# Optimization experiments

Hardware: AMD Instinct MI355X
Metric: run time of the kernel (lower is better)

## Reference

```python
import jax, jax.numpy as jnp
import numpy as np

B, N, M = 8, 1024, 64          # graphs, ops/graph, machines/graph
OPF, MF = 16, 8                # raw feature dims
H, D, L = 8, 64, 3             # heads, head dim, HGT layers
F = H * D                      # 512 = hidden_dim * num_heads
KC = 8                         # compatible machines per op
NOP, NM = B * N, B * M
EPS = 1e-5


def _graph_ln(x, w, b):
    # PyG LayerNorm(mode='graph') with batch=None: scalar mean/std over the whole tensor
    x = x - x.mean()
    return x / (x.std() + EPS) * w + b


def _seg_softmax(a, idx, n):
    amax = jax.ops.segment_max(a, idx, num_segments=n)
    amax = jnp.where(jnp.isfinite(amax), amax, 0.0)
    ex = jnp.exp(a - amax[idx])
    s = jax.ops.segment_sum(ex, idx, num_segments=n)
    return ex / (s[idx] + 1e-16)


def _forward(op_x, machine_x, W_emb_op, b_emb_op, W_emb_m, b_emb_m,
             opn_w, opn_b, mn_w, mn_b, Wk, bk, Wq, bq, Wv, bv,
             A_rel, M_rel, p_rel, W_out, b_out, skip, ln_w, ln_b,
             ei_precedes, ei_canproc, ei_compat):
    x_op = _graph_ln(op_x @ W_emb_op + b_emb_op, opn_w, opn_b)
    x_m = _graph_ln(machine_x @ W_emb_m + b_emb_m, mn_w, mn_b)
    s0, d0 = ei_precedes   # op -> op
    s1, d1 = ei_canproc    # machine -> op
    s2, d2 = ei_compat     # op -> machine
    scale = 1.0 / jnp.sqrt(jnp.float32(D))
    for l in range(L):
        k_op = (x_op @ Wk[l, 0] + bk[l, 0]).reshape(NOP, H, D)
        q_op = (x_op @ Wq[l, 0] + bq[l, 0]).reshape(NOP, H, D)
        v_op = (x_op @ Wv[l, 0] + bv[l, 0]).reshape(NOP, H, D)
        k_m = (x_m @ Wk[l, 1] + bk[l, 1]).reshape(NM, H, D)
        q_m = (x_m @ Wq[l, 1] + bq[l, 1]).reshape(NM, H, D)
        v_m = (x_m @ Wv[l, 1] + bv[l, 1]).reshape(NM, H, D)
        # relation-specific per-head transforms (a_rel/m_rel of HGTConv)
        k0 = jnp.einsum('nhd,hde->nhe', k_op, A_rel[l, 0]); v0 = jnp.einsum('nhd,hde->nhe', v_op, M_rel[l, 0])
        k1 = jnp.einsum('nhd,hde->nhe', k_m, A_rel[l, 1]);  v1 = jnp.einsum('nhd,hde->nhe', v_m, M_rel[l, 1])
        k2 = jnp.einsum('nhd,hde->nhe', k_op, A_rel[l, 2]); v2 = jnp.einsum('nhd,hde->nhe', v_op, M_rel[l, 2])
        # attention into op nodes: joint softmax over both incoming edge types
        a0 = (q_op[d0] * k0[s0]).sum(-1) * p_rel[l, 0] * scale   # [E0,H]
        a1 = (q_op[d1] * k1[s1]).sum(-1) * p_rel[l, 1] * scale   # [E1,H]
        a_op = jnp.concatenate([a0, a1]); dd = jnp.concatenate([d0, d1])
        w = _seg_softmax(a_op, dd, NOP)
        msg = jnp.concatenate([v0[s0], v1[s1]]) * w[:, :, None]
        agg_op = jax.ops.segment_sum(msg, dd, num_segments=NOP).reshape(NOP, F)
        # attention into machine nodes
        a2 = (q_m[d2] * k2[s2]).sum(-1) * p_rel[l, 2] * scale
        w2 = _seg_softmax(a2, d2, NM)
        agg_m = jax.ops.segment_sum(v2[s2] * w2[:, :, None], d2, num_segments=NM).reshape(NM, F)
        # output projection + learned skip gate (HGTConv internals)
        o_op = jax.nn.gelu(agg_op, approximate=False) @ W_out[l, 0] + b_out[l, 0]
        o_m = jax.nn.gelu(agg_m, approximate=False) @ W_out[l, 1] + b_out[l, 1]
        g_op = jax.nn.sigmoid(skip[l, 0]); g_m = jax.nn.sigmoid(skip[l, 1])
        o_op = g_op * o_op + (1.0 - g_op) * x_op
        o_m = g_m * o_m + (1.0 - g_m) * x_m
        # wrapper residual + dropout(eval=identity) + graph layer norm
        x_op = _graph_ln(o_op + x_op, ln_w[l], ln_b[l])
        x_m = _graph_ln(o_m + x_m, ln_w[l], ln_b[l])
    fea_j = x_op.reshape(B, N, F)
    fea_m = x_m.reshape(B, M, F)
    return fea_j, fea_m, fea_j.mean(1, keepdims=True), fea_m.mean(1, keepdims=True)


def setup_inputs() -> dict:
    key = jax.random.key(0)
    ks = jax.random.split(key, 12)
    rng = np.random.default_rng(0)
    ids = np.arange(NOP).reshape(B, N)
    src0 = ids[:, :-1].ravel(); dst0 = ids[:, 1:].ravel()
    mach = rng.integers(0, M, size=(B, N, KC)) + (np.arange(B) * M)[:, None, None]
    ops = np.broadcast_to(ids[:, :, None], (B, N, KC))
    ei_precedes = jnp.asarray(np.stack([src0, dst0]), dtype=jnp.int32)
    ei_canproc = jnp.asarray(np.stack([mach.ravel(), ops.ravel()]), dtype=jnp.int32)
    ei_compat = jnp.asarray(np.stack([ops.ravel(), mach.ravel()]), dtype=jnp.int32)
    n = lambda k, sh, s=0.05: jax.random.normal(k, sh, dtype=jnp.float32) * s
    return dict(
        op_x=n(ks[0], (NOP, OPF), 1.0),
        machine_x=n(ks[1], (NM, MF), 1.0),
        W_emb_op=n(ks[2], (OPF, F)), b_emb_op=jnp.zeros((F,), jnp.float32),
        W_emb_m=n(ks[3], (MF, F)), b_emb_m=jnp.zeros((F,), jnp.float32),
        opn_w=jnp.ones((F,), jnp.float32), opn_b=jnp.zeros((F,), jnp.float32),
        mn_w=jnp.ones((F,), jnp.float32), mn_b=jnp.zeros((F,), jnp.float32),
        Wk=n(ks[4], (L, 2, F, F)), bk=jnp.zeros((L, 2, F), jnp.float32),
        Wq=n(ks[5], (L, 2, F, F)), bq=jnp.zeros((L, 2, F), jnp.float32),
        Wv=n(ks[6], (L, 2, F, F)), bv=jnp.zeros((L, 2, F), jnp.float32),
        A_rel=n(ks[7], (L, 3, H, D, D)), M_rel=n(ks[8], (L, 3, H, D, D)),
        p_rel=jnp.ones((L, 3, H), jnp.float32),
        W_out=n(ks[9], (L, 2, F, F)), b_out=jnp.zeros((L, 2, F), jnp.float32),
        skip=jnp.ones((L, 2), jnp.float32),
        ln_w=jnp.ones((L, F), jnp.float32), ln_b=jnp.zeros((L, F), jnp.float32),
        ei_precedes=ei_precedes, ei_canproc=ei_canproc, ei_compat=ei_compat,
    )


def reference(op_x, machine_x, W_emb_op, b_emb_op, W_emb_m, b_emb_m,
              opn_w, opn_b, mn_w, mn_b, Wk, bk, Wq, bq, Wv, bv,
              A_rel, M_rel, p_rel, W_out, b_out, skip, ln_w, ln_b,
              ei_precedes, ei_canproc, ei_compat):
    return _forward(op_x, machine_x, W_emb_op, b_emb_op, W_emb_m, b_emb_m,
                    opn_w, opn_b, mn_w, mn_b, Wk, bk, Wq, bq, Wv, bv,
                    A_rel, M_rel, p_rel, W_out, b_out, skip, ln_w, ln_b,
                    ei_precedes, ei_canproc, ei_compat)
```

## Files before the change

kernel.cpp:

```cpp
#include <hip/hip_runtime.h>

typedef unsigned short u16;
typedef __attribute__((ext_vector_type(4))) float floatx4;
typedef __attribute__((ext_vector_type(8))) short shortx8;
typedef __attribute__((ext_vector_type(4))) short shortx4;

#define NOPS 8192
#define NMS  512
#define CQ   2560
#define CM   1536
#define NE2  65536
#define TOPC (NOPS*512)
#define TMC  (NMS*512)

__device__ __forceinline__ float bf2f(u16 u){ return __uint_as_float(((unsigned)u)<<16); }
__device__ __forceinline__ u16 f2bf(float f){
  unsigned u = __float_as_uint(f);
  u += 0x7FFFu + ((u>>16)&1u);
  return (u16)(u>>16);
}
__device__ __forceinline__ float wred(float v){
  #pragma unroll
  for (int o=32;o;o>>=1) v += __shfl_xor(v,o,64);
  return v;
}
__device__ __forceinline__ float wredmax(float v){
  #pragma unroll
  for (int o=32;o;o>>=1) v = fmaxf(v, __shfl_xor(v,o,64));
  return v;
}
__device__ __forceinline__ float geluf(float x){
  return 0.5f*x*(1.f+erff(x*0.70710678118654752f));
}
__device__ __forceinline__ void block_stat_out2(float s, float s2, float* pstat, int slot){
  __shared__ float sb[8];
  s = wred(s); s2 = wred(s2);
  int wv = threadIdx.x >> 6;
  if ((threadIdx.x & 63) == 0){ sb[wv*2] = s; sb[wv*2+1] = s2; }
  __syncthreads();
  if (threadIdx.x == 0){
    float a = 0.f, b = 0.f;
    int nw = blockDim.x >> 6;
    for (int i=0;i<nw;++i){ a += sb[i*2]; b += sb[i*2+1]; }
    pstat[slot*2]   = a;
    pstat[slot*2+1] = b;
  }
}

__global__ __launch_bounds__(256) void cnt2_k(const int* __restrict__ s1, float* __restrict__ Ct,
                                              float* __restrict__ Cn){
  int idx = blockIdx.x*256 + threadIdx.x;
  int n = idx >> 6, l = idx & 63;
  const int* row = s1 + n*8;
  int cnt = 0;
  #pragma unroll
  for (int j=0;j<8;++j) cnt += ((row[j] & 63) == l);
  float f = (float)cnt;
  Cn[(size_t)n*64 + l] = f;
  int b = n >> 10, nl = n & 1023;
  Ct[(size_t)((b<<6) + l)*1024 + nl] = f;
}

__global__ __launch_bounds__(256) void twout_k(const float* __restrict__ src, u16* __restrict__ dst){
  __shared__ u16 t[64][65];
  int l = blockIdx.x, kb = blockIdx.y*64, nb = blockIdx.z*64;
  const float* s = src + (size_t)l*262144;
  u16* d = dst + (size_t)l*262144;
  int tx = threadIdx.x & 63, ty4 = threadIdx.x >> 6;
  #pragma unroll 4
  for (int p=0;p<16;++p){
    int k = ty4 + p*4;
    t[k][tx] = f2bf(s[(size_t)(kb+k)*512 + nb + tx]);
  }
  __syncthreads();
  #pragma unroll 4
  for (int p=0;p<16;++p){
    int n = ty4 + p*4;
    d[(size_t)(nb+n)*512 + kb + tx] = t[tx][n];
  }
}

__global__ __launch_bounds__(256) void tq_k(const float* __restrict__ Wq,
                                            u16* __restrict__ Wc_op_t, u16* __restrict__ Wc_m_t){
  __shared__ u16 tl[64][65];
  int blk = blockIdx.x;
  int l = blk >> 1, side = blk & 1;
  const float* s = Wq + (size_t)blk*262144;
  u16* d = side ? (Wc_m_t + (size_t)l*CM*512) : (Wc_op_t + (size_t)l*CQ*512);
  int kb = blockIdx.y*64, nb = blockIdx.z*64;
  int tx = threadIdx.x & 63, ty4 = threadIdx.x >> 6;
  #pragma unroll 4
  for (int p=0;p<16;++p){
    int k = ty4 + p*4;
    tl[k][tx] = f2bf(s[(size_t)(kb+k)*512 + nb + tx]);
  }
  __syncthreads();
  #pragma unroll 4
  for (int p=0;p<16;++p){
    int n = ty4 + p*4;
    d[(size_t)(nb+n)*512 + kb + tx] = tl[tx][n];
  }
}

__global__ void qb_k(const float* __restrict__ bq, float* bias_op, float* bias_m){
  int i = blockIdx.x*blockDim.x + threadIdx.x;
  if (i >= 3072) return;
  int l = i >> 10, side = (i >> 9) & 1, f = i & 511;
  float v = bq[(l*2+side)*512 + f];
  if (side==0) bias_op[l*CQ + f] = v; else bias_m[l*CM + f] = v;
}

__global__ __launch_bounds__(256) void combine3_k(const float* __restrict__ Wk, const float* __restrict__ Wv,
                                                  const float* __restrict__ Ar, const float* __restrict__ Mr,
                                                  u16* __restrict__ Wc_op_t, u16* __restrict__ Wc_m_t){
  __shared__ u16 As[64*72];
  __shared__ u16 Bs[128*72];
  int gx = blockIdx.x;
  int l = gx/48; int rem = gx - l*48; int s = rem >> 3; int h = rem & 7;
  int side = (s < 4) ? 0 : 1;
  int r = (s < 4) ? (s+1) : (s-3);
  int useK = side==0 ? (s==0 || s==2) : (s==4);
  int rel  = side==0 ? ((s<2)?0:2) : 1;
  const float* W   = (useK ? Wk : Wv) + (size_t)(l*2+side)*262144;
  const float* Rel = (useK ? Ar : Mr) + ((size_t)(l*3+rel)*8 + h)*4096;
  int h64 = h*64;
  u16* Wt = side ? (Wc_m_t + (size_t)l*CM*512) : (Wc_op_t + (size_t)l*CQ*512);
  int rbase = r*512 + h64;
  int cc0 = blockIdx.y * 128;
  int tid = threadIdx.x, lane = tid & 63, wave = tid >> 6;
  {
    int d = tid >> 2, e0 = (tid & 3) * 16;
    #pragma unroll
    for (int j=0;j<16;++j) As[(e0+j)*72 + d] = f2bf(Rel[d*64 + e0 + j]);
  }
  {
    int ccl = tid >> 1, d0 = (tid & 1) * 32;
    const float* src = W + (size_t)(cc0+ccl)*512 + h64 + d0;
    #pragma unroll
    for (int j=0;j<32;j+=4){
      floatx4 v = *(const floatx4*)(src + j);
      shortx4 sv;
      #pragma unroll
      for (int e=0;e<4;++e) sv[e] = (short)f2bf(v[e]);
      *(shortx4*)(Bs + ccl*72 + d0 + j) = sv;
    }
  }
  __syncthreads();
  int wm = wave & 1, wn = wave >> 1;
  int mrow = lane & 15, quad = lane >> 4;
  floatx4 acc[2][4];
  #pragma unroll
  for (int a=0;a<2;++a)
    #pragma unroll
    for (int b=0;b<4;++b) acc[a][b] = (floatx4){0.f,0.f,0.f,0.f};
  #pragma unroll
  for (int ks=0; ks<2; ++ks){
    shortx8 af[2], bf[4];
    #pragma unroll
    for (int mt=0;mt<2;++mt) af[mt] = *(const shortx8*)(As + (wm*32 + mt*16 + mrow)*72 + ks*32 + quad*8);
    #pragma unroll
    for (int nt=0;nt<4;++nt) bf[nt] = *(const shortx8*)(Bs + (wn*64 + nt*16 + mrow)*72 + ks*32 + quad*8);
    #pragma unroll
    for (int mt=0;mt<2;++mt)
      #pragma unroll
      for (int nt=0;nt<4;++nt)
        acc[mt][nt] = __builtin_amdgcn_mfma_f32_16x16x32_bf16(af[mt], bf[nt], acc[mt][nt], 0, 0, 0);
  }
  #pragma unroll
  for (int mt=0;mt<2;++mt){
    #pragma unroll
    for (int nt=0;nt<4;++nt){
      int ccl = wn*64 + nt*16 + mrow;
      #pragma unroll
      for (int r2=0;r2<4;++r2){
        int e = wm*32 + mt*16 + quad*4 + r2;
        Wt[(size_t)(rbase + e)*512 + cc0 + ccl] = f2bf(acc[mt][nt][r2]);
      }
    }
  }
}
__global__ void cbias_k(const float* __restrict__ bk, const float* __restrict__ bv,
                        const float* __restrict__ Ar, const float* __restrict__ Mr,
                        float* bias_op, float* bias_m){
  int gx = blockIdx.x; int e = threadIdx.x;
  int l = gx/48; int rem = gx - l*48; int s = rem >> 3; int h = rem & 7;
  int side = (s < 4) ? 0 : 1;
  int r = (s < 4) ? (s+1) : (s-3);
  int useK = side==0 ? (s==0 || s==2) : (s==4);
  int rel  = side==0 ? ((s<2)?0:2) : 1;
  const float* bb  = (useK ? bk : bv) + (size_t)(l*2+side)*512 + h*64;
  const float* Rel = (useK ? Ar : Mr) + ((size_t)(l*3+rel)*8 + h)*4096;
  float acc = 0.f;
  for (int d=0; d<64; ++d) acc += bb[d]*Rel[d*64 + e];
  float* bias = side ? (bias_m + l*CM) : (bias_op + l*CQ);
  bias[r*512 + h*64 + e] = acc;
}

__global__ __launch_bounds__(256) void embed2_k(const float* __restrict__ Xop, const float* __restrict__ Wop,
                                                const float* __restrict__ bop, float* __restrict__ Yop,
                                                const float* __restrict__ Xm, const float* __restrict__ Wm,
                                                const float* __restrict__ bm_, float* __restrict__ Ym,
                                                float* pstat, float* pstat_m){
  int bid = blockIdx.x;
  const float *X, *W, *bias; float *Y, *ps; int K, total, nb, lb;
  if (bid < 1024){ X=Xop; W=Wop; bias=bop; Y=Yop; ps=pstat;   K=16; total=TOPC; nb=1024; lb=bid; }
  else           { X=Xm;  W=Wm;  bias=bm_; Y=Ym;  ps=pstat_m; K=8;  total=TMC;  nb=128;  lb=bid-1024; }
  float s = 0.f, s2 = 0.f;
  for (int idx = lb*256 + threadIdx.x; idx < total; idx += nb*256){
    int n = idx >> 9, f = idx & 511;
    float v = bias[f];
    for (int c=0;c<K;++c) v += X[n*K+c] * W[c*512+f];
    Y[idx] = v;
    s += v; s2 += v*v;
  }
  block_stat_out2(s, s2, ps, lb);
}

__global__ __launch_bounds__(256) void ln2_k(const float* __restrict__ src_op, float* __restrict__ dst_op,
                                             u16* __restrict__ dbf_op, const float* __restrict__ w_op,
                                             const float* __restrict__ b_op,
                                             const float* __restrict__ src_m, float* __restrict__ dst_m,
                                             u16* __restrict__ dbf_m, const float* __restrict__ w_m,
                                             const float* __restrict__ b_m,
                                             const float* __restrict__ pstat, const float* __restrict__ pstat_m){
  int bid = blockIdx.x;
  const float *src, *w, *b, *ps; float* dst; u16* dbf; int total4, nb, lb, nblk; float inv_n;
  if (bid < 1024){ src=src_op; dst=dst_op; dbf=dbf_op; w=w_op; b=b_op; ps=pstat;
                   total4=TOPC/4; nb=1024; lb=bid; nblk=1024; inv_n=1.f/TOPC; }
  else           { src=src_m;  dst=dst_m;  dbf=dbf_m;  w=w_m;  b=b_m;  ps=pstat_m;
                   total4=TMC/4;  nb=128;  lb=bid-1024; nblk=128; inv_n=1.f/TMC; }
  __shared__ float sb[8];
  __shared__ float mr[2];
  float s = 0.f, s2 = 0.f;
  for (int i = threadIdx.x; i < nblk; i += 256){ s += ps[2*i]; s2 += ps[2*i+1]; }
  s = wred(s); s2 = wred(s2);
  int wv = threadIdx.x >> 6;
  if ((threadIdx.x & 63) == 0){ sb[wv*2] = s; sb[wv*2+1] = s2; }
  __syncthreads();
  if (threadIdx.x == 0){
    float a = 0.f, bsum = 0.f;
    for (int i=0;i<4;++i){ a += sb[i*2]; bsum += sb[i*2+1]; }
    float mean = a * inv_n;
    float var  = fmaxf(bsum * inv_n - mean*mean, 0.f);
    mr[0] = mean;
    mr[1] = 1.f/(sqrtf(var) + 1e-5f);
  }
  __syncthreads();
  float mean = mr[0], rinv = mr[1];
  const floatx4* s4 = (const floatx4*)src;
  floatx4* d4 = (floatx4*)dst;
  shortx4* db4 = (shortx4*)dbf;
  const floatx4* w4 = (const floatx4*)w;
  const floatx4* b4 = (const floatx4*)b;
  for (int i = lb*256 + threadIdx.x; i < total4; i += nb*256){
    int f = i & 127;
    floatx4 v = s4[i], wv2 = w4[f], bv = b4[f];
    shortx4 sv;
    #pragma unroll
    for (int e=0;e<4;++e){ v[e] = (v[e]-mean)*rinv*wv2[e] + bv[e]; sv[e] = (short)f2bf(v[e]); }
    d4[i] = v;
    db4[i] = sv;
  }
}

__global__ __launch_bounds__(256) void gate2_k(float* __restrict__ y_op, const float* __restrict__ x_op,
                                               const float* __restrict__ bo_op, const float* __restrict__ sk_op,
                                               float* __restrict__ y_m, const float* __restrict__ x_m,
                                               const float* __restrict__ bo_m, const float* __restrict__ sk_m,
                                               float* pstat, float* pstat_m){
  int bid = blockIdx.x;
  float *y, *ps; const float *x, *bo, *sk; int total4, nb, lb;
  if (bid < 1024){ y=y_op; x=x_op; bo=bo_op; sk=sk_op; ps=pstat;   total4=TOPC/4; nb=1024; lb=bid; }
  else           { y=y_m;  x=x_m;  bo=bo_m;  sk=sk_m;  ps=pstat_m; total4=TMC/4;  nb=128;  lb=bid-1024; }
  float g = 1.f/(1.f+expf(-(*sk)));
  floatx4* y4 = (floatx4*)y;
  const floatx4* x4 = (const floatx4*)x;
  const floatx4* b4 = (const floatx4*)bo;
  float s = 0.f, s2 = 0.f;
  for (int i = lb*256 + threadIdx.x; i < total4; i += nb*256){
    floatx4 yv = y4[i], xv = x4[i], bv = b4[i & 127];
    #pragma unroll
    for (int e=0;e<4;++e){
      float o = g*(yv[e]+bv[e]) + (2.f-g)*xv[e];
      yv[e] = o;
      s += o; s2 += o*o;
    }
    y4[i] = yv;
  }
  block_stat_out2(s, s2, ps, lb);
}

__device__ __forceinline__ void gemm_core(u16* As, u16* Bs, const u16* __restrict__ A,
                                          const u16* __restrict__ Bt, const float* __restrict__ bias,
                                          void* __restrict__ Cp, int N, int K, int out_bf16,
                                          int bx, int by){
  const int tid = threadIdx.x;
  const int lane = tid & 63, wave = tid >> 6;
  const int bm = by * 128, bn = bx * 128;
  const int wm = wave & 1, wn = wave >> 1;
  const int mrow = lane & 15, quad = lane >> 4;
  const u16* Ab = A + (size_t)bm*K;
  const u16* Bb = Bt + (size_t)bn*K;
  floatx4 acc[4][4];
  #pragma unroll
  for (int a=0;a<4;++a)
    #pragma unroll
    for (int b=0;b<4;++b) acc[a][b] = (floatx4){0.f,0.f,0.f,0.f};
  const int r0 = tid >> 2, c0 = (tid & 3) * 8;
  const int r1 = (tid+256) >> 2, c1 = ((tid+256) & 3) * 8;
  const int lds0 = wave*512;
  const int lds1 = wave*512 + 2048;
  for (int k0 = 0; k0 < K; k0 += 32){
    __builtin_amdgcn_global_load_lds((const __attribute__((address_space(1))) void*)(Ab + (size_t)r0*K + k0 + c0),
                                     (__attribute__((address_space(3))) void*)(As + lds0), 16, 0, 0);
    __builtin_amdgcn_global_load_lds((const __attribute__((address_space(1))) void*)(Ab + (size_t)r1*K + k0 + c1),
                                     (__attribute__((address_space(3))) void*)(As + lds1), 16, 0, 0);
    __builtin_amdgcn_global_load_lds((const __attribute__((address_space(1))) void*)(Bb + (size_t)r0*K + k0 + c0),
                                     (__attribute__((address_space(3))) void*)(Bs + lds0), 16, 0, 0);
    __builtin_amdgcn_global_load_lds((const __attribute__((address_space(1))) void*)(Bb + (size_t)r1*K + k0 + c1),
                                     (__attribute__((address_space(3))) void*)(Bs + lds1), 16, 0, 0);
    __syncthreads();
    shortx8 af[4], bf[4];
    #pragma unroll
    for (int mt=0;mt<4;++mt) af[mt] = *(const shortx8*)(As + (wm*64 + mt*16 + mrow)*32 + quad*8);
    #pragma unroll
    for (int nt=0;nt<4;++nt) bf[nt] = *(const shortx8*)(Bs + (wn*64 + nt*16 + mrow)*32 + quad*8);
    #pragma unroll
    for (int mt=0;mt<4;++mt)
      #pragma unroll
      for (int nt=0;nt<4;++nt)
        acc[mt][nt] = __builtin_amdgcn_mfma_f32_16x16x32_bf16(af[mt], bf[nt], acc[mt][nt], 0, 0, 0);
    __syncthreads();
  }
  #pragma unroll
  for (int mt=0;mt<4;++mt){
    #pragma unroll
    for (int nt=0;nt<4;++nt){
      int col = bn + wn*64 + nt*16 + mrow;
      float bval = bias ? bias[col] : 0.f;
      #pragma unroll
      for (int r2=0;r2<4;++r2){
        int row = bm + wm*64 + mt*16 + quad*4 + r2;
        float v = acc[mt][nt][r2] + bval;
        if (out_bf16) ((u16*)Cp)[(size_t)row*N + col] = f2bf(v);
        else          ((float*)Cp)[(size_t)row*N + col] = v;
      }
    }
  }
}
__global__ __launch_bounds__(256) void gemm2_k(const u16* A1, const u16* B1, const float* bias1, void* C1,
                                               int N1, int ob1, int ntx1, int nblk1,
                                               const u16* A2, const u16* B2, const float* bias2, void* C2,
                                               int N2, int ob2, int ntx2, int K){
  __shared__ u16 As[128*32];
  __shared__ u16 Bs[128*32];
  int id = blockIdx.x;
  if (id < nblk1) gemm_core(As, Bs, A1, B1, bias1, C1, N1, K, ob1, id % ntx1, id / ntx1);
  else { int j = id - nblk1; gemm_core(As, Bs, A2, B2, bias2, C2, N2, K, ob2, j % ntx2, j / ntx2); }
}

__global__ __launch_bounds__(256) void qk12_k(const u16* __restrict__ qkv_op, const u16* __restrict__ qkv_m,
                                              const float* __restrict__ prel, const float* __restrict__ Cn,
                                              u16* __restrict__ W1, float* __restrict__ wpre,
                                              float* __restrict__ linv, float* __restrict__ S2f){
  __shared__ __align__(16) char smem[36864];
  u16* As = (u16*)smem;
  u16* Bs = As + 128*72;
  float* Sbuf = (float*)smem;
  int bh = blockIdx.y; int b = bh >> 3, h = bh & 7;
  int n0 = blockIdx.x * 128;
  int tid = threadIdx.x, lane = tid & 63, wave = tid >> 6;
  int mrow = lane & 15, quad = lane >> 4;
  if (blockIdx.z == 0){
    int wm = wave & 1, wn = wave >> 1;
    float p1 = prel[8 + h] * 0.125f;
    {
      int row = tid >> 1, col = (tid & 1) * 32;
      const u16* src = qkv_op + (size_t)(b*1024 + n0 + row)*CQ + h*64 + col;
      #pragma unroll
      for (int e=0;e<4;++e) *(shortx8*)(As + row*72 + col + e*8) = *(const shortx8*)(src + e*8);
    }
    {
      int row = tid >> 2, col = (tid & 3) * 16;
      const u16* src = qkv_m + (size_t)(b*64 + row)*CM + 512 + h*64 + col;
      *(shortx8*)(Bs + row*72 + col)     = *(const shortx8*)(src);
      *(shortx8*)(Bs + row*72 + col + 8) = *(const shortx8*)(src + 8);
    }
    __syncthreads();
    floatx4 acc[4][2];
    #pragma unroll
    for (int a=0;a<4;++a){ acc[a][0] = (floatx4){0,0,0,0}; acc[a][1] = (floatx4){0,0,0,0}; }
    #pragma unroll
    for (int ks=0; ks<2; ++ks){
      shortx8 af[4], bf[2];
      #pragma unroll
      for (int mt=0;mt<4;++mt) af[mt] = *(const shortx8*)(As + (wm*64 + mt*16 + mrow)*72 + ks*32 + quad*8);
      #pragma unroll
      for (int nt=0;nt<2;++nt) bf[nt] = *(const shortx8*)(Bs + (wn*32 + nt*16 + mrow)*72 + ks*32 + quad*8);
      #pragma unroll
      for (int mt=0;mt<4;++mt)
        #pragma unroll
        for (int nt=0;nt<2;++nt)
          acc[mt][nt] = __builtin_amdgcn_mfma_f32_16x16x32_bf16(af[mt], bf[nt], acc[mt][nt], 0, 0, 0);
    }
    __syncthreads();
    #pragma unroll
    for (int mt=0;mt<4;++mt){
      #pragma unroll
      for (int nt=0;nt<2;++nt){
        int m = wn*32 + nt*16 + mrow;
        #pragma unroll
        for (int r2=0;r2<4;++r2){
          int nl = wm*64 + mt*16 + quad*4 + r2;
          Sbuf[nl*65 + m] = acc[mt][nt][r2] * p1;
        }
      }
    }
    __syncthreads();
    if (tid < 128){
      int n_g = b*1024 + n0 + tid;
      int nl  = n0 + tid;
      float sp = -1e30f;
      if (nl > 0){
        float p0 = prel[h] * 0.125f;
        const u16* qp = qkv_op + (size_t)n_g*CQ + h*64;
        const u16* kp = qkv_op + (size_t)(n_g-1)*CQ + 512 + h*64;
        float d = 0.f;
        #pragma unroll
        for (int j=0;j<8;++j){
          shortx8 qa = *(const shortx8*)(qp + j*8);
          shortx8 ka = *(const shortx8*)(kp + j*8);
          #pragma unroll
          for (int e=0;e<8;++e) d += bf2f((u16)qa[e])*bf2f((u16)ka[e]);
        }
        sp = d * p0;
      }
      const float* crow = Cn + (size_t)n_g*64;
      float mx = sp;
      #pragma unroll
      for (int m=0;m<64;++m){
        if (crow[m] > 0.f) mx = fmaxf(mx, Sbuf[tid*65 + m]);
      }
      float L = 0.f;
      u16* wrow = W1 + ((size_t)n_g*8 + h)*64;
      #pragma unroll
      for (int m0=0;m0<64;m0+=4){
        shortx4 pv;
        #pragma unroll
        for (int e=0;e<4;++e){
          float c = crow[m0+e];
          float w = (c > 0.f) ? c*expf(Sbuf[tid*65 + m0+e]-mx) : 0.f;
          L += w;
          pv[e] = (short)f2bf(w);
        }
        *(shortx4*)(wrow + m0) = pv;
      }
      float ep = (nl > 0) ? expf(sp - mx) : 0.f;
      L += ep;
      wpre[(size_t)n_g*8 + h] = ep;
      linv[(size_t)n_g*8 + h] = 1.f/(L + 1e-16f);
    }
  } else {
    float p2 = prel[16 + h] * 0.125f;
    {
      int row = tid >> 2, col = (tid & 3) * 16;
      const u16* src = qkv_m + (size_t)(b*64+row)*CM + h*64 + col;
      *(shortx8*)(As + row*72 + col)     = *(const shortx8*)(src);
      *(shortx8*)(As + row*72 + col + 8) = *(const shortx8*)(src + 8);
    }
    {
      int row = tid >> 1, col = (tid & 1) * 32;
      const u16* src = qkv_op + (size_t)(b*1024 + n0 + row)*CQ + 1536 + h*64 + col;
      #pragma unroll
      for (int e=0;e<4;++e) *(shortx8*)(Bs + row*72 + col + e*8) = *(const shortx8*)(src + e*8);
    }
    __syncthreads();
    floatx4 acc[4][2];
    #pragma unroll
    for (int a=0;a<4;++a){ acc[a][0] = (floatx4){0,0,0,0}; acc[a][1] = (floatx4){0,0,0,0}; }
    #pragma unroll
    for (int ks=0; ks<2; ++ks){
      shortx8 af[4], bf[2];
      #pragma unroll
      for (int mt=0;mt<4;++mt) af[mt] = *(const shortx8*)(As + (mt*16 + mrow)*72 + ks*32 + quad*8);
      #pragma unroll
      for (int nt=0;nt<2;++nt) bf[nt] = *(const shortx8*)(Bs + (wave*32 + nt*16 + mrow)*72 + ks*32 + quad*8);
      #pragma unroll
      for (int mt=0;mt<4;++mt)
        #pragma unroll
        for (int nt=0;nt<2;++nt)
          acc[mt][nt] = __builtin_amdgcn_mfma_f32_16x16x32_bf16(af[mt], bf[nt], acc[mt][nt], 0, 0, 0);
    }
    #pragma unroll
    for (int mt=0;mt<4;++mt){
      #pragma unroll
      for (int nt=0;nt<2;++nt){
        int n = n0 + wave*32 + nt*16 + mrow;
        #pragma unroll
        for (int r2=0;r2<4;++r2){
          int m = mt*16 + quad*4 + r2;
          S2f[((size_t)(b*64 + m)*8 + h)*1024 + n] = acc[mt][nt][r2] * p2;
        }
      }
    }
  }
}

__global__ __launch_bounds__(512) void msoftm_k(const float* __restrict__ S2f, const float* __restrict__ Ct,
                                                u16* __restrict__ W2){
  int m = blockIdx.x;
  int h = threadIdx.x >> 6, d = threadIdx.x & 63;
  const float* srow = S2f + ((size_t)m*8 + h)*1024;
  const float* crow = Ct + (size_t)m*1024;
  float s[16], c[16];
  #pragma unroll
  for (int it=0; it<16; ++it){ s[it] = srow[it*64 + d]; c[it] = crow[it*64 + d]; }
  float mx = -1e30f;
  #pragma unroll
  for (int it=0; it<16; ++it) if (c[it] > 0.f) mx = fmaxf(mx, s[it]);
  mx = wredmax(mx);
  float e[16], L = 0.f;
  #pragma unroll
  for (int it=0; it<16; ++it){
    e[it] = (c[it] > 0.f) ? c[it]*expf(s[it]-mx) : 0.f;
    L += e[it];
  }
  L = wred(L);
  float inv = 1.f/(L + 1e-16f);
  u16* wrow = W2 + ((size_t)m*8 + h)*1024;
  #pragma unroll
  for (int it=0; it<16; ++it) wrow[it*64 + d] = f2bf(e[it]*inv);
}

__global__ __launch_bounds__(256) void agg12_k(const u16* __restrict__ W1, const u16* __restrict__ qkv_op,
                                               const u16* __restrict__ qkv_m, const float* __restrict__ wpre,
                                               const float* __restrict__ linv, u16* __restrict__ agg_op,
                                               const u16* __restrict__ W2, u16* __restrict__ agg_m){
  __shared__ u16 As[128*72];
  __shared__ u16 Bs[64*72];
  int bid = blockIdx.x;
  int tid = threadIdx.x, lane = tid & 63, wave = tid >> 6;
  int wm = wave & 1, wn = wave >> 1;
  int mrow = lane & 15, quad = lane >> 4;
  if (bid < 512){
    int bh = bid >> 3; int b = bh >> 3, h = bh & 7;
    int n0 = (bid & 7) * 128;
    {
      int row = tid >> 1, col = (tid & 1) * 32;
      const u16* src = W1 + ((size_t)(b*1024 + n0 + row)*8 + h)*64 + col;
      #pragma unroll
      for (int e=0;e<4;++e) *(shortx8*)(As + row*72 + col + e*8) = *(const shortx8*)(src + e*8);
    }
    {
      int m = tid >> 2, dcol = (tid & 3) * 16;
      const u16* src = qkv_m + (size_t)(b*64 + m)*CM + 1024 + h*64 + dcol;
      shortx8 v0 = *(const shortx8*)(src);
      shortx8 v1 = *(const shortx8*)(src + 8);
      #pragma unroll
      for (int e=0;e<8;++e){ Bs[(dcol+e)*72 + m] = (u16)v0[e]; Bs[(dcol+8+e)*72 + m] = (u16)v1[e]; }
    }
    __syncthreads();
    floatx4 acc[4][2];
    #pragma unroll
    for (int a=0;a<4;++a){ acc[a][0] = (floatx4){0,0,0,0}; acc[a][1] = (floatx4){0,0,0,0}; }
    #pragma unroll
    for (int ks=0; ks<2; ++ks){
      shortx8 af[4], bf[2];
      #pragma unroll
      for (int mt=0;mt<4;++mt) af[mt] = *(const shortx8*)(As + (wm*64 + mt*16 + mrow)*72 + ks*32 + quad*8);
      #pragma unroll
      for (int nt=0;nt<2;++nt) bf[nt] = *(const shortx8*)(Bs + (wn*32 + nt*16 + mrow)*72 + ks*32 + quad*8);
      #pragma unroll
      for (int mt=0;mt<4;++mt)
        #pragma unroll
        for (int nt=0;nt<2;++nt)
          acc[mt][nt] = __builtin_amdgcn_mfma_f32_16x16x32_bf16(af[mt], bf[nt], acc[mt][nt], 0, 0, 0);
    }
    #pragma unroll
    for (int mt=0;mt<4;++mt){
      #pragma unroll
      for (int nt=0;nt<2;++nt){
        int d = wn*32 + nt*16 + mrow;
        #pragma unroll
        for (int r2=0;r2<4;++r2){
          int n = n0 + wm*64 + mt*16 + quad*4 + r2;
          size_t ng = (size_t)b*1024 + n;
          size_t ih = ng*8 + h;
          float v = acc[mt][nt][r2];
          if ((n & 1023) > 0) v += wpre[ih] * bf2f(qkv_op[(ng-1)*CQ + 1024 + h*64 + d]);
          v *= linv[ih];
          agg_op[ng*512 + h*64 + d] = f2bf(geluf(v));
        }
      }
    }
  } else {
    int bh = bid - 512; int b = bh >> 3, h = bh & 7;
    floatx4 acc[2][2];
    acc[0][0]=(floatx4){0,0,0,0}; acc[0][1]=(floatx4){0,0,0,0};
    acc[1][0]=(floatx4){0,0,0,0}; acc[1][1]=(floatx4){0,0,0,0};
    const int arow = tid >> 2, acol = (tid & 3) * 8;
    const int nrow = tid >> 3, dcol = (tid & 7) * 8;
    for (int ks = 0; ks < 32; ++ks){
      int nn0 = ks*32;
      *(shortx8*)(As + arow*40 + acol) =
          *(const shortx8*)(W2 + ((size_t)(b*64 + arow)*8 + h)*1024 + nn0 + acol);
      shortx8 vv = *(const shortx8*)(qkv_op + (size_t)(b*1024 + nn0 + nrow)*CQ + 2048 + h*64 + dcol);
      #pragma unroll
      for (int e=0;e<8;++e) Bs[(dcol+e)*40 + nrow] = (u16)vv[e];
      __syncthreads();
      shortx8 af[2], bf[2];
      #pragma unroll
      for (int mt=0;mt<2;++mt) af[mt] = *(const shortx8*)(As + (wm*32 + mt*16 + mrow)*40 + quad*8);
      #pragma unroll
      for (int nt=0;nt<2;++nt) bf[nt] = *(const shortx8*)(Bs + (wn*32 + nt*16 + mrow)*40 + quad*8);
      #pragma unroll
      for (int mt=0;mt<2;++mt)
        #pragma unroll
        for (int nt=0;nt<2;++nt)
          acc[mt][nt] = __builtin_amdgcn_mfma_f32_16x16x32_bf16(af[mt], bf[nt], acc[mt][nt], 0, 0, 0);
      __syncthreads();
    }
    #pragma unroll
    for (int mt=0;mt<2;++mt){
      #pragma unroll
      for (int nt=0;nt<2;++nt){
        int dd = wn*32 + nt*16 + mrow;
        #pragma unroll
        for (int r2=0;r2<4;++r2){
          int m = wm*32 + mt*16 + quad*4 + r2;
          agg_m[(size_t)(b*64 + m)*512 + h*64 + dd] = f2bf(geluf(acc[mt][nt][r2]));
        }
      }
    }
  }
}

__global__ __launch_bounds__(512) void meanj_part_k(const float* __restrict__ xo, float* scratchJ){
  int b = blockIdx.x, chunk = blockIdx.y, f = threadIdx.x;
  float s = 0.f;
  for (int r=0;r<128;++r){
    int row = b*1024 + chunk*128 + r;
    s += xo[(size_t)row*512 + f];
  }
  scratchJ[(b*8 + chunk)*512 + f] = s;
}
__global__ __launch_bounds__(512) void mean2_k(const float* __restrict__ scratchJ, float* __restrict__ out){
  int i = blockIdx.x*512 + threadIdx.x;
  if (i < 4096){
    int b = i >> 9, f = i & 511;
    float s = 0.f;
    #pragma unroll
    for (int c=0;c<8;++c) s += scratchJ[(b*8+c)*512 + f];
    out[4456448 + i] = s * (1.f/1024.f);
  } else {
    int j = i - 4096;
    int b = j >> 9, f = j & 511;
    float s = 0.f;
    for (int r=0;r<64;++r) s += out[(size_t)TOPC + (size_t)(b*64+r)*512 + f];
    out[4460544 + j] = s * (1.f/64.f);
  }
}

extern "C" void kernel_launch(void* const* d_in, const int* in_sizes, int n_in,
                              void* d_out, int out_size, void* d_ws, size_t ws_size,
                              hipStream_t stream){
  const float* op_x      = (const float*)d_in[0];
  const float* machine_x = (const float*)d_in[1];
  const float* W_emb_op  = (const float*)d_in[2];
  const float* b_emb_op  = (const float*)d_in[3];
  const float* W_emb_m   = (const float*)d_in[4];
  const float* b_emb_m   = (const float*)d_in[5];
  const float* opn_w     = (const float*)d_in[6];
  const float* opn_b     = (const float*)d_in[7];
  const float* mn_w      = (const float*)d_in[8];
  const float* mn_b      = (const float*)d_in[9];
  const float* Wk        = (const float*)d_in[10];
  const float* bk        = (const float*)d_in[11];
  const float* Wq        = (const float*)d_in[12];
  const float* bq        = (const float*)d_in[13];
  const float* Wv        = (const float*)d_in[14];
  const float* bv        = (const float*)d_in[15];
  const float* A_rel     = (const float*)d_in[16];
  const float* M_rel     = (const float*)d_in[17];
  const float* p_rel     = (const float*)d_in[18];
  const float* W_out     = (const float*)d_in[19];
  const float* b_out     = (const float*)d_in[20];
  const float* skip      = (const float*)d_in[21];
  const float* ln_w      = (const float*)d_in[22];
  const float* ln_b      = (const float*)d_in[23];
  const int* s1          = (const int*)d_in[25];
  float* out = (float*)d_out;

  char* ws = (char*)d_ws;
  size_t off = 0;
  auto alloc = [&](size_t bytes)->void*{
    void* p = ws + off;
    off = (off + bytes + 255) & ~(size_t)255;
    return p;
  };
  float* pstat     = (float*)alloc(4096*4);
  float* scratchJ  = (float*)alloc(32768*4);
  float* Ct        = (float*)alloc((size_t)NMS*1024*4);
  float* Cn        = (float*)alloc((size_t)NOPS*64*4);
  float* S2f       = (float*)alloc((size_t)NMS*8*1024*4);
  u16*   W2        = (u16*)  alloc((size_t)NMS*8*1024*2);
  u16*   W1        = (u16*)  alloc((size_t)NOPS*8*64*2);
  float* wpre      = (float*)alloc((size_t)NOPS*8*4);
  float* linv      = (float*)alloc((size_t)NOPS*8*4);
  float* x_op      = (float*)alloc((size_t)NOPS*512*4);
  u16*   x_op_bf   = (u16*)  alloc((size_t)NOPS*512*2);
  float* x_m       = (float*)alloc((size_t)NMS*512*4);
  u16*   x_m_bf    = (u16*)  alloc((size_t)NMS*512*2);
  u16*   qkv_op    = (u16*)  alloc((size_t)NOPS*CQ*2);
  u16*   qkv_m     = (u16*)  alloc((size_t)NMS*CM*2);
  u16*   agg_op    = (u16*)  alloc((size_t)NOPS*512*2);
  u16*   agg_m     = (u16*)  alloc((size_t)NMS*512*2);
  u16*   Wc_op_t   = (u16*)  alloc((size_t)3*CQ*512*2);
  float* bias_op   = (float*)alloc((size_t)3*CQ*4);
  u16*   Wc_m_t    = (u16*)  alloc((size_t)3*CM*512*2);
  float* bias_m    = (float*)alloc((size_t)3*CM*4);
  u16*   Wout_t    = (u16*)  alloc((size_t)6*262144*2);
  float* o_op      = (float*)qkv_op;
  float* o_m       = (float*)qkv_m;
  float* pstat_m   = pstat + 2048;

  cnt2_k<<<2048,256,0,stream>>>(s1, Ct, Cn);
  twout_k<<<dim3(6,8,8),256,0,stream>>>(W_out, Wout_t);
  tq_k<<<dim3(6,8,8),256,0,stream>>>(Wq, Wc_op_t, Wc_m_t);
  qb_k<<<12,256,0,stream>>>(bq, bias_op, bias_m);
  combine3_k<<<dim3(144,4),256,0,stream>>>(Wk, Wv, A_rel, M_rel, Wc_op_t, Wc_m_t);
  cbias_k<<<144,64,0,stream>>>(bk, bv, A_rel, M_rel, bias_op, bias_m);

  embed2_k<<<1152,256,0,stream>>>(op_x, W_emb_op, b_emb_op, x_op,
                                  machine_x, W_emb_m, b_emb_m, x_m, pstat, pstat_m);
  ln2_k<<<1152,256,0,stream>>>(x_op, x_op, x_op_bf, opn_w, opn_b,
                               x_m, x_m, x_m_bf, mn_w, mn_b, pstat, pstat_m);

  for (int l=0; l<3; ++l){
    int last = (l == 2);
    gemm2_k<<<1328,256,0,stream>>>(x_op_bf, Wc_op_t + (size_t)l*CQ*512, bias_op + l*CQ, qkv_op, CQ, 1, 20, 1280,
                                   x_m_bf, Wc_m_t + (size_t)l*CM*512, bias_m + l*CM, qkv_m, CM, 1, 12, 512);
    qk12_k<<<dim3(8,64,2),256,0,stream>>>(qkv_op, qkv_m, p_rel + l*24, Cn, W1, wpre, linv, S2f);
    msoftm_k<<<NMS,512,0,stream>>>(S2f, Ct, W2);
    agg12_k<<<576,256,0,stream>>>(W1, qkv_op, qkv_m, wpre, linv, agg_op, W2, agg_m);
    gemm2_k<<<272,256,0,stream>>>(agg_op, Wout_t + (size_t)(l*2+0)*262144, nullptr, o_op, 512, 0, 4, 256,
                                  agg_m, Wout_t + (size_t)(l*2+1)*262144, nullptr, o_m, 512, 0, 4, 512);
    gate2_k<<<1152,256,0,stream>>>(o_op, x_op, b_out + (size_t)(l*2+0)*512, skip + l*2+0,
                                   o_m, x_m, b_out + (size_t)(l*2+1)*512, skip + l*2+1, pstat, pstat_m);
    ln2_k<<<1152,256,0,stream>>>(o_op, last ? out : x_op, x_op_bf, ln_w + l*512, ln_b + l*512,
                                 o_m, last ? (out + TOPC) : x_m, x_m_bf, ln_w + l*512, ln_b + l*512,
                                 pstat, pstat_m);
  }

  meanj_part_k<<<dim3(8,8),512,0,stream>>>(out, scratchJ);
  mean2_k<<<16,512,0,stream>>>(scratchJ, out);
}
```

Before: 630.9 us.

## Replace QKV projection GEMM with 256x256-tile pipelined direct-to-LDS kernel

Adds a new 512-thread GEMM kernel with 256x256 output tiles, swizzled global_load_lds staging into a double-buffered 128KB LDS region, and an interleaved schedule that overlaps loads of the next K chunk with MFMA work using barriers and setprio. It replaces the 128x128-tile gemm2_k for the per-layer QKV projection. The aim is more operand reuse per LDS byte and better latency hiding. In exchange there are far fewer blocks (332), a large LDS footprint that limits occupancy, and fragile hand-written waitcnt sequencing.

```diff
diff --git a/kernel.cpp b/kernel.cpp
--- a/kernel.cpp
+++ b/kernel.cpp
@@ -357,6 +357,127 @@
   int id = blockIdx.x;
   if (id < nblk1) gemm_core(As, Bs, A1, B1, bias1, C1, N1, K, ob1, id % ntx1, id / ntx1);
   else { int j = id - nblk1; gemm_core(As, Bs, A2, B2, bias2, C2, N2, K, ob2, j % ntx2, j / ntx2); }
+}
+
+__device__ __forceinline__ void stage_half8(const u16* __restrict__ src, int kc, u16* region, int tid){
+  int wave = tid >> 6;
+  #pragma unroll
+  for (int j=0;j<2;++j){
+    int idx = j*512 + tid;
+    int row = idx >> 2, qp2 = idx & 3;
+    int qs = qp2 ^ (((row >> 3) & 1) << 1);
+    __builtin_amdgcn_global_load_lds(
+      (const __attribute__((address_space(1))) void*)(src + (size_t)row*512 + kc + qs*8),
+      (__attribute__((address_space(3))) void*)(region + (j*512 + wave*64)*8),
+      16, 0, 0);
+  }
+}
+
+#define MFMA_QUAD(MH) do { \
+  __builtin_amdgcn_s_barrier(); \
+  asm volatile("s_waitcnt lgkmcnt(0)" ::: "memory"); \
+  __builtin_amdgcn_sched_barrier(0); \
+  __builtin_amdgcn_s_setprio(1); \
+  _Pragma("unroll") \
+  for (int mt=0;mt<4;++mt){ \
+    _Pragma("unroll") \
+    for (int nt=0;nt<4;++nt) \
+      acc[(MH)*4+mt][nt] = __builtin_amdgcn_mfma_f32_16x16x32_bf16(af[mt], bf[nt], acc[(MH)*4+mt][nt], 0, 0, 0); \
+  } \
+  __builtin_amdgcn_s_setprio(0); \
+} while(0)
+
+__global__ __launch_bounds__(512, 2) void gemm8_k(
+    const u16* __restrict__ A1, const u16* __restrict__ B1, const float* __restrict__ bias1,
+    u16* __restrict__ C1, int N1, int nbx1, int nblk1,
+    const u16* __restrict__ A2, const u16* __restrict__ B2, const float* __restrict__ bias2,
+    u16* __restrict__ C2, int N2, int nbx2){
+  extern __shared__ u16 lds[];
+  int id = blockIdx.x;
+  const u16 *A, *Bt; const float* bias; u16* C; int N, bx, by;
+  if (id < nblk1){ A=A1; Bt=B1; bias=bias1; C=C1; N=N1; bx=id%nbx1; by=id/nbx1; }
+  else { int j=id-nblk1; A=A2; Bt=B2; bias=bias2; C=C2; N=N2; bx=j%nbx2; by=j/nbx2; }
+  const int tid = threadIdx.x, lane = tid & 63, wave = tid >> 6;
+  const int wm = wave & 1, wn = wave >> 1;
+  const int mrow = lane & 15, quad = lane >> 4;
+  const int qp = quad ^ ((mrow & 8) ? 2 : 0);
+  const u16* Ab = A + (size_t)(by*256)*512;
+  const u16* Bb = Bt + (size_t)(bx*256)*512;
+
+  floatx4 acc[8][4];
+  #pragma unroll
+  for (int a=0;a<8;++a)
+    #pragma unroll
+    for (int b=0;b<4;++b) acc[a][b] = (floatx4){0.f,0.f,0.f,0.f};
+
+  stage_half8(Ab, 0,  lds,          tid);
+  stage_half8(Bb, 0,  lds + 16384,  tid);
+  stage_half8(Ab, 32, lds + 8192,   tid);
+  stage_half8(Bb, 32, lds + 24576,  tid);
+  stage_half8(Ab, 64, lds + 32768,  tid);
+  stage_half8(Bb, 64, lds + 49152,  tid);
+  asm volatile("s_waitcnt vmcnt(4)" ::: "memory");
+  __builtin_amdgcn_s_barrier();
+
+  for (int t = 0; t < 8; ++t){
+    const int s = t & 1;
+    u16* Sbase = lds + s*32768;
+    u16* Obase = lds + (s^1)*32768;
+    const u16* a0 = Sbase + (wm*128 + mrow)*32 + qp*8;
+    const u16* b0 = Sbase + 16384 + (wn*64 + mrow)*32 + qp*8;
+    const int kc1 = (t+1)*64, kc2 = (t+2)*64;
+    shortx8 af[4], bf[4];
+
+    #pragma unroll
+    for (int mt=0;mt<4;++mt) af[mt] = *(const shortx8*)(a0 + mt*512);
+    #pragma unroll
+    for (int nt=0;nt<4;++nt) bf[nt] = *(const shortx8*)(b0 + nt*512);
+    if (t < 7) stage_half8(Ab, kc1 + 32, Obase + 8192, tid);
+    MFMA_QUAD(0);
+    __builtin_amdgcn_s_barrier();
+
+    #pragma unroll
+    for (int mt=0;mt<4;++mt) af[mt] = *(const shortx8*)(a0 + 2048 + mt*512);
+    if (t < 7) stage_half8(Bb, kc1 + 32, Obase + 24576, tid);
+    MFMA_QUAD(1);
+    __builtin_amdgcn_s_barrier();
+
+    #pragma unroll
+    for (int mt=0;mt<4;++mt) af[mt] = *(const shortx8*)(a0 + 8192 + mt*512);
+    #pragma unroll
+    for (int nt=0;nt<4;++nt) bf[nt] = *(const shortx8*)(b0 + 8192 + nt*512);
+    if (t < 6) stage_half8(Ab, kc2, Sbase, tid);
+    MFMA_QUAD(0);
+    __builtin_amdgcn_s_barrier();
+
+    #pragma unroll
+    for (int mt=0;mt<4;++mt) af[mt] = *(const shortx8*)(a0 + 8192 + 2048 + mt*512);
+    if (t < 6) stage_half8(Bb, kc2, Sbase + 16384, tid);
+    MFMA_QUAD(1);
+    if (t < 6) asm volatile("s_waitcnt vmcnt(4)" ::: "memory");
+    else       asm volatile("s_waitcnt vmcnt(0)" ::: "memory");
+    __builtin_amdgcn_s_barrier();
+  }
+
+  const int crow0 = by*256 + wm*128 + quad*4;
+  const int ccol0 = bx*256 + wn*64 + mrow;
+  float bv[4];
+  #pragma unroll
+  for (int nt=0;nt<4;++nt) bv[nt] = bias ? bias[ccol0 + nt*16] : 0.f;
+  #pragma unroll
+  for (int mh=0;mh<2;++mh){
+    #pragma unroll
+    for (int mt=0;mt<4;++mt){
+      int row = crow0 + mh*64 + mt*16;
+      #pragma unroll
+      for (int nt=0;nt<4;++nt){
+        int col = ccol0 + nt*16;
+        #pragma unroll
+        for (int r2=0;r2<4;++r2)
+          C[(size_t)(row+r2)*N + col] = f2bf(acc[mh*4+mt][nt][r2] + bv[nt]);
+      }
+    }
+  }
 }
 
 __global__ __launch_bounds__(256) void qk12_k(const u16* __restrict__ qkv_op, const u16* __restrict__ qkv_m,
@@ -738,8 +859,8 @@
 
   for (int l=0; l<3; ++l){
     int last = (l == 2);
-    gemm2_k<<<1328,256,0,stream>>>(x_op_bf, Wc_op_t + (size_t)l*CQ*512, bias_op + l*CQ, qkv_op, CQ, 1, 20, 1280,
-                                   x_m_bf, Wc_m_t + (size_t)l*CM*512, bias_m + l*CM, qkv_m, CM, 1, 12, 512);
+    gemm8_k<<<332,512,131072,stream>>>(x_op_bf, Wc_op_t + (size_t)l*CQ*512, bias_op + l*CQ, qkv_op, CQ, 10, 320,
+                                       x_m_bf, Wc_m_t + (size_t)l*CM*512, bias_m + l*CM, qkv_m, CM, 6);
     qk12_k<<<dim3(8,64,2),256,0,stream>>>(qkv_op, qkv_m, p_rel + l*24, Cn, W1, wpre, linv, S2f);
     msoftm_k<<<NMS,512,0,stream>>>(S2f, Ct, W2);
     agg12_k<<<576,256,0,stream>>>(W1, qkv_op, qkv_m, wpre, linv, agg_op, W2, agg_m);
```

Result: faster. 612.9 us (-2.8%).
